# Kernel optimization log

Measured on AMD Instinct MI355X. Metric: run time of the kernel, lower is better.

The kernel has to match this reference:

```python
import jax, jax.numpy as jnp
import numpy as np

INPUT_DIM = 512
HIDDEN_DIM = 1024


def glorot_normal(key, shape):
    fan_in, fan_out = shape[0], shape[1]
    std = jnp.sqrt(2.0 / (fan_in + fan_out))
    return std * jax.random.normal(key, shape, dtype=jnp.float32)


def setup_inputs() -> dict:
    key = jax.random.key(0)
    k1, k2, k3 = jax.random.split(key, 3)
    b, t = 32, 1024
    H = HIDDEN_DIM + INPUT_DIM
    x_btd = jax.random.normal(k1, (b, t, INPUT_DIM), dtype=jnp.float32)
    input_paddings = jnp.zeros((b, t), dtype=jnp.float32)
    kernel = glorot_normal(k2, (H, 4 * HIDDEN_DIM))  # [H, 4h]
    bias = jnp.zeros((4 * HIDDEN_DIM,), dtype=jnp.float32)
    h_init = glorot_normal(k3, (1, HIDDEN_DIM))
    return {"x_btd": x_btd, "input_paddings": input_paddings,
            "kernel": kernel, "bias": bias, "h_init": h_init}


def lstm_step(carry, x_bd, kernel, bias):
    h_bh, c_bh = carry
    x_bH = jnp.concatenate([x_bd, h_bh], axis=-1)          # [b, d+h]
    gate_out = jnp.einsum('bH,Hh->bh', x_bH, kernel) + bias  # [b, 4h]
    f, i, o, g = jnp.split(gate_out, 4, axis=-1)
    c_new = jax.nn.sigmoid(f) * c_bh + jax.nn.sigmoid(i) * jnp.tanh(g)
    h_new = jax.nn.sigmoid(o) * jnp.tanh(c_new)
    return (h_new, c_new), h_new


def reference(x_btd, input_paddings, kernel, bias, h_init) -> jnp.ndarray:
    del input_paddings
    b = x_btd.shape[0]
    h0 = jnp.tile(h_init, (b, 1))                # [b, h]
    c0 = jnp.zeros((b, HIDDEN_DIM), dtype=x_btd.dtype)
    x_tbd = jnp.transpose(x_btd, (1, 0, 2))      # [t, b, d]

    def step(carry, x_bd):
        return lstm_step(carry, x_bd, kernel, bias)

    _, h_tbh = jax.lax.scan(step, (h0, c0), x_tbd)
    return jnp.transpose(h_tbh, (1, 0, 2))       # [b, t, h]
```

## Files before the change

### kernel.cpp

```cpp
#include <hip/hip_runtime.h>


#define T_STEPS 1024
#define BATCH   32
#define DIN     512
#define HID     1024
#define KTOT    1536
#define NBLK    128
#define WCOLS   32
#define WSTR    1544
#define REDSTR  33
#define REDW    (32*REDSTR)

#define LDS_W_BYTES   (WCOLS*WSTR*2)
#define LDS_RED_BYTES (4*REDW*4)
#define LDS_TOTAL     (LDS_W_BYTES + LDS_RED_BYTES)

typedef __attribute__((ext_vector_type(8))) short  short8;
typedef __attribute__((ext_vector_type(4))) float  floatx4;
typedef __attribute__((ext_vector_type(4))) unsigned short ushort4_;

__device__ __forceinline__ unsigned short f2bf(float f) {
    unsigned u = __builtin_bit_cast(unsigned, f);
    u += 0x7FFFu + ((u >> 16) & 1u);
    return (unsigned short)(u >> 16);
}
__device__ __forceinline__ float sigf(float x) { return 1.f / (1.f + __expf(-x)); }

__device__ __forceinline__ floatx4 coh_load16(const void* p) {
    floatx4 v;
    asm volatile("global_load_dwordx4 %0, %1, off sc0 sc1" : "=v"(v) : "v"(p));
    return v;
}
__device__ __forceinline__ int coh_load4(const void* p) {
    int v;
    asm volatile("global_load_dword %0, %1, off sc0 sc1\n\ts_waitcnt vmcnt(0)"
                 : "=v"(v) : "v"(p) : "memory");
    return v;
}
__device__ __forceinline__ void coh_store2(void* p, unsigned short v) {
    asm volatile("global_store_short %0, %1, off sc0 sc1" :: "v"(p), "v"((unsigned)v) : "memory");
}
__device__ __forceinline__ void coh_store4(void* p, int v) {
    asm volatile("global_store_dword %0, %1, off sc0 sc1" :: "v"(p), "v"(v) : "memory");
}
__device__ __forceinline__ void wait_vm0() {
    asm volatile("s_waitcnt vmcnt(0)" ::: "memory");
}

__global__ __launch_bounds__(256) void prep_wt(const float* __restrict__ kern,
                                               unsigned short* __restrict__ wt) {
    __shared__ unsigned short tile[64][72];
    const int c0 = (blockIdx.x & 63) * 64;
    const int k0 = (blockIdx.x >> 6) * 64;
    const int cl = threadIdx.x & 63;
    const int kg = threadIdx.x >> 6;
    #pragma unroll
    for (int i = 0; i < 16; ++i) {
        int kl = kg * 16 + i;
        tile[cl][kl] = f2bf(kern[(k0 + kl) * 4096 + c0 + cl]);
    }
    __syncthreads();
    #pragma unroll
    for (int i = 0; i < 16; ++i) {
        int cc = kg * 16 + i;
        wt[(size_t)(c0 + cc) * KTOT + k0 + cl] = tile[cc][cl];
    }
}

__global__ __launch_bounds__(256) void prep_x(const float* __restrict__ x,
                                              unsigned short* __restrict__ xT) {
    const int row = blockIdx.x * 2 + (threadIdx.x >> 7);
    const int l   = threadIdx.x & 127;
    const int b = row >> 10, t = row & 1023;
    float4 v = ((const float4*)(x + (size_t)row * DIN))[l];
    ushort4_ o;
    o.x = f2bf(v.x); o.y = f2bf(v.y); o.z = f2bf(v.z); o.w = f2bf(v.w);
    *(ushort4_*)(xT + ((size_t)t * BATCH + b) * DIN + l * 4) = o;
}

__global__ __launch_bounds__(256) void init_h(const float* __restrict__ h_init,
                                              unsigned short* __restrict__ hbuf,
                                              int* __restrict__ flags) {
    if (blockIdx.x == 32) {
        if (threadIdx.x < NBLK) flags[threadIdx.x] = 0;
        return;
    }
    const int b = blockIdx.x;
    for (int u = threadIdx.x; u < HID; u += 256)
        hbuf[b * HID + u] = f2bf(h_init[u]);
}

__global__ __launch_bounds__(256, 1) void lstm_persist(
    const unsigned short* __restrict__ wt,
    const unsigned short* __restrict__ xT,
    unsigned short* __restrict__ hbuf,
    int* __restrict__ flags,
    const float* __restrict__ bias,
    float* __restrict__ out)
{
    extern __shared__ char smem[];
    unsigned short* ldsW = (unsigned short*)smem;
    float* red = (float*)(smem + LDS_W_BYTES);

    const int bk   = blockIdx.x;
    const int tid  = threadIdx.x;
    const int wave = tid >> 6;
    const int lane = tid & 63;
    const int lrow = lane & 15;
    const int kq   = lane >> 4;

    for (int cl = wave; cl < WCOLS; cl += 4) {
        const int gcol = (cl >> 3) * HID + bk * 8 + (cl & 7);
        const unsigned short* src = wt + (size_t)gcol * KTOT;
        unsigned short* dst = ldsW + cl * WSTR;
        for (int k = lane * 8; k < KTOT; k += 512)
            *(short8*)(dst + k) = *(const short8*)(src + k);
    }

    const int pb = tid >> 3;
    const int pu = tid & 7;
    float bias_r[4];
    #pragma unroll
    for (int g = 0; g < 4; ++g) bias_r[g] = bias[g * HID + bk * 8 + pu];
    float c_state = 0.f;
    __syncthreads();

    for (int t = 0; t < T_STEPS; ++t) {
        floatx4 zero = {0.f, 0.f, 0.f, 0.f};
        floatx4 acc[2][2];
        acc[0][0] = zero; acc[0][1] = zero; acc[1][0] = zero; acc[1][1] = zero;

        const unsigned short* xb = xT + (size_t)t * (BATCH * DIN);
        #pragma unroll
        for (int i = 0; i < 4; ++i) {
            const int kl = wave * 128 + i * 32 + kq * 8;
            short8 a0 = *(const short8*)(xb + lrow * DIN + kl);
            short8 a1 = *(const short8*)(xb + (lrow + 16) * DIN + kl);
            short8 b0 = *(const short8*)(ldsW + lrow * WSTR + kl);
            short8 b1 = *(const short8*)(ldsW + (lrow + 16) * WSTR + kl);
            acc[0][0] = __builtin_amdgcn_mfma_f32_16x16x32_bf16(a0, b0, acc[0][0], 0, 0, 0);
            acc[0][1] = __builtin_amdgcn_mfma_f32_16x16x32_bf16(a0, b1, acc[0][1], 0, 0, 0);
            acc[1][0] = __builtin_amdgcn_mfma_f32_16x16x32_bf16(a1, b0, acc[1][0], 0, 0, 0);
            acc[1][1] = __builtin_amdgcn_mfma_f32_16x16x32_bf16(a1, b1, acc[1][1], 0, 0, 0);
        }

        if (t > 0 && tid < NBLK) {
            const int* fl = flags + tid;
            while (coh_load4(fl) < t)
                __builtin_amdgcn_s_sleep(1);
        }
        __syncthreads();

        const unsigned short* hb = hbuf + (size_t)(t & 1) * (BATCH * HID);
        floatx4 ha[8][2];
        #pragma unroll
        for (int i = 0; i < 8; ++i) {
            const int kh = wave * 256 + i * 32 + kq * 8;
            ha[i][0] = coh_load16(hb + lrow * HID + kh);
            ha[i][1] = coh_load16(hb + (lrow + 16) * HID + kh);
        }
        wait_vm0();
        #pragma unroll
        for (int i = 0; i < 8; ++i) {
            const int kw = 512 + wave * 256 + i * 32 + kq * 8;
            short8 a0 = __builtin_bit_cast(short8, ha[i][0]);
            short8 a1 = __builtin_bit_cast(short8, ha[i][1]);
            short8 b0 = *(const short8*)(ldsW + lrow * WSTR + kw);
            short8 b1 = *(const short8*)(ldsW + (lrow + 16) * WSTR + kw);
            acc[0][0] = __builtin_amdgcn_mfma_f32_16x16x32_bf16(a0, b0, acc[0][0], 0, 0, 0);
            acc[0][1] = __builtin_amdgcn_mfma_f32_16x16x32_bf16(a0, b1, acc[0][1], 0, 0, 0);
            acc[1][0] = __builtin_amdgcn_mfma_f32_16x16x32_bf16(a1, b0, acc[1][0], 0, 0, 0);
            acc[1][1] = __builtin_amdgcn_mfma_f32_16x16x32_bf16(a1, b1, acc[1][1], 0, 0, 0);
        }

        #pragma unroll
        for (int mt = 0; mt < 2; ++mt)
            #pragma unroll
            for (int nt = 0; nt < 2; ++nt)
                #pragma unroll
                for (int r = 0; r < 4; ++r) {
                    const int row = mt * 16 + kq * 4 + r;
                    const int col = nt * 16 + lrow;
                    red[wave * REDW + row * REDSTR + col] = acc[mt][nt][r];
                }
        __syncthreads();

        float gv[4];
        #pragma unroll
        for (int g = 0; g < 4; ++g) {
            const int col = g * 8 + pu;
            float s = bias_r[g];
            #pragma unroll
            for (int w = 0; w < 4; ++w) s += red[w * REDW + pb * REDSTR + col];
            gv[g] = s;
        }
        const float fg = sigf(gv[0]);
        const float ig = sigf(gv[1]);
        const float og = sigf(gv[2]);
        const float gg = tanhf(gv[3]);
        c_state = fg * c_state + ig * gg;
        const float hn = og * tanhf(c_state);

        out[(size_t)pb * (T_STEPS * HID) + (size_t)t * HID + bk * 8 + pu] = hn;
        unsigned short* hp = hbuf + (size_t)((t + 1) & 1) * (BATCH * HID)
                                  + pb * HID + bk * 8 + pu;
        coh_store2(hp, f2bf(hn));

        wait_vm0();
        __syncthreads();
        if (tid == 0)
            coh_store4(flags + bk, t + 1);
    }
}

extern "C" void kernel_launch(void* const* d_in, const int* in_sizes, int n_in,
                              void* d_out, int out_size, void* d_ws, size_t ws_size,
                              hipStream_t stream) {
    (void)in_sizes; (void)n_in; (void)out_size;
    const float* x      = (const float*)d_in[0];
    const float* kern   = (const float*)d_in[2];
    const float* bias   = (const float*)d_in[3];
    const float* h_init = (const float*)d_in[4];
    float* out = (float*)d_out;

    char* ws = (char*)d_ws;
    unsigned short* wt    = (unsigned short*)(ws);
    unsigned short* xT    = (unsigned short*)(ws + 12582912);
    unsigned short* hbuf  = (unsigned short*)(ws + 12582912 + 33554432);
    int*            flags = (int*)(ws + 12582912 + 33554432 + 131072);
    (void)ws_size;

    hipFuncSetAttribute((const void*)lstm_persist,
                        hipFuncAttributeMaxDynamicSharedMemorySize, LDS_TOTAL);

    prep_wt<<<dim3(64 * 24), dim3(256), 0, stream>>>(kern, wt);
    prep_x<<<dim3(BATCH * T_STEPS / 2), dim3(256), 0, stream>>>(x, xT);
    init_h<<<dim3(33), dim3(256), 0, stream>>>(h_init, hbuf, flags);

    void* args[] = { &wt, &xT, &hbuf, &flags, &bias, &out };
    hipLaunchCooperativeKernel((const void*)lstm_persist, dim3(NBLK), dim3(256),
                               args, LDS_TOTAL, stream);
}
```

Before: 5.329 ms.

## Stage h in LDS for vector stores, pad flags, per-wave flag polling

Each block now writes its new hidden-state slice into LDS, and one wave publishes it with 16-byte stores per batch row. This replaces 256 separate 2-byte coherent stores. The per-block flags are padded to a 16-byte stride. Each wave now polls only the 32 producer flags whose h slice it actually reads, which removes the block-wide barrier before the h loads. The sc0 bit is also dropped from the coherent loads and stores to use a cheaper cache scope, which carries some risk to cross-block visibility semantics.

```diff
diff --git a/kernel.cpp b/kernel.cpp
--- a/kernel.cpp
+++ b/kernel.cpp
@@ -14,7 +14,8 @@
 
 #define LDS_W_BYTES   (WCOLS*WSTR*2)
 #define LDS_RED_BYTES (4*REDW*4)
-#define LDS_TOTAL     (LDS_W_BYTES + LDS_RED_BYTES)
+#define LDS_H_BYTES   (256*2)
+#define LDS_TOTAL     (LDS_W_BYTES + LDS_RED_BYTES + LDS_H_BYTES)
 
 typedef __attribute__((ext_vector_type(8))) short  short8;
 typedef __attribute__((ext_vector_type(4))) float  floatx4;
@@ -29,20 +30,20 @@
 
 __device__ __forceinline__ floatx4 coh_load16(const void* p) {
     floatx4 v;
-    asm volatile("global_load_dwordx4 %0, %1, off sc0 sc1" : "=v"(v) : "v"(p));
+    asm volatile("global_load_dwordx4 %0, %1, off sc1" : "=v"(v) : "v"(p));
     return v;
 }
 __device__ __forceinline__ int coh_load4(const void* p) {
     int v;
-    asm volatile("global_load_dword %0, %1, off sc0 sc1\n\ts_waitcnt vmcnt(0)"
+    asm volatile("global_load_dword %0, %1, off sc1\n\ts_waitcnt vmcnt(0)"
                  : "=v"(v) : "v"(p) : "memory");
     return v;
 }
-__device__ __forceinline__ void coh_store2(void* p, unsigned short v) {
-    asm volatile("global_store_short %0, %1, off sc0 sc1" :: "v"(p), "v"((unsigned)v) : "memory");
+__device__ __forceinline__ void coh_store16(void* p, short8 v) {
+    asm volatile("global_store_dwordx4 %0, %1, off sc1" :: "v"(p), "v"(v) : "memory");
 }
 __device__ __forceinline__ void coh_store4(void* p, int v) {
-    asm volatile("global_store_dword %0, %1, off sc0 sc1" :: "v"(p), "v"(v) : "memory");
+    asm volatile("global_store_dword %0, %1, off sc1" :: "v"(p), "v"(v) : "memory");
 }
 __device__ __forceinline__ void wait_vm0() {
     asm volatile("s_waitcnt vmcnt(0)" ::: "memory");
@@ -83,7 +84,7 @@
                                               unsigned short* __restrict__ hbuf,
                                               int* __restrict__ flags) {
     if (blockIdx.x == 32) {
-        if (threadIdx.x < NBLK) flags[threadIdx.x] = 0;
+        for (int i = threadIdx.x; i < NBLK * 4; i += 256) flags[i] = 0;
         return;
     }
     const int b = blockIdx.x;
@@ -102,6 +103,7 @@
     extern __shared__ char smem[];
     unsigned short* ldsW = (unsigned short*)smem;
     float* red = (float*)(smem + LDS_W_BYTES);
+    unsigned short* hLDS = (unsigned short*)(smem + LDS_W_BYTES + LDS_RED_BYTES);
 
     const int bk   = blockIdx.x;
     const int tid  = threadIdx.x;
@@ -124,6 +126,8 @@
     #pragma unroll
     for (int g = 0; g < 4; ++g) bias_r[g] = bias[g * HID + bk * 8 + pu];
     float c_state = 0.f;
+
+    const int* myflag = flags + (wave * 32 + (lane & 31)) * 4;
     __syncthreads();
 
     for (int t = 0; t < T_STEPS; ++t) {
@@ -145,12 +149,10 @@
             acc[1][1] = __builtin_amdgcn_mfma_f32_16x16x32_bf16(a1, b1, acc[1][1], 0, 0, 0);
         }
 
-        if (t > 0 && tid < NBLK) {
-            const int* fl = flags + tid;
-            while (coh_load4(fl) < t)
+        if (t > 0) {
+            while (coh_load4(myflag) < t)
                 __builtin_amdgcn_s_sleep(1);
         }
-        __syncthreads();
 
         const unsigned short* hb = hbuf + (size_t)(t & 1) * (BATCH * HID);
         floatx4 ha[8][2];
@@ -203,14 +205,20 @@
         const float hn = og * tanhf(c_state);
 
         out[(size_t)pb * (T_STEPS * HID) + (size_t)t * HID + bk * 8 + pu] = hn;
-        unsigned short* hp = hbuf + (size_t)((t + 1) & 1) * (BATCH * HID)
-                                  + pb * HID + bk * 8 + pu;
-        coh_store2(hp, f2bf(hn));
-
-        wait_vm0();
+        hLDS[tid] = f2bf(hn);
         __syncthreads();
-        if (tid == 0)
-            coh_store4(flags + bk, t + 1);
+
+        if (wave == 0) {
+            if (lane < 32) {
+                short8 v = *(const short8*)(hLDS + lane * 8);
+                unsigned short* hp = hbuf + (size_t)((t + 1) & 1) * (BATCH * HID)
+                                          + lane * HID + bk * 8;
+                coh_store16(hp, v);
+            }
+            wait_vm0();
+            if (lane == 0)
+                coh_store4(flags + bk * 4, t + 1);
+        }
     }
 }
 
```

Result: faster. 5.020 ms (-5.8%).

## Replace per-block flag barrier with tag bits embedded in hidden-state values

Applied to the files above, without the earlier changes.

Removes the per-step flag polling and flag stores. Each bf16 hidden value now carries its LSB as a parity tag for the step, and consumers spin-reload only the h vectors whose tags do not match yet. This drops the separate flag round trip, the extra vmcnt wait before the flag store, and the s_sleep polling latency from the recurrent critical path. The cost is one bit of bf16 mantissa precision in h, plus reliance on 16-bit stores staying atomic and visible with sc1 only (sc0 is dropped). The reduction stride also changes.

```diff
diff --git a/kernel.cpp b/kernel.cpp
--- a/kernel.cpp
+++ b/kernel.cpp
@@ -9,7 +9,7 @@
 #define NBLK    128
 #define WCOLS   32
 #define WSTR    1544
-#define REDSTR  33
+#define REDSTR  35
 #define REDW    (32*REDSTR)
 
 #define LDS_W_BYTES   (WCOLS*WSTR*2)
@@ -18,6 +18,7 @@
 
 typedef __attribute__((ext_vector_type(8))) short  short8;
 typedef __attribute__((ext_vector_type(4))) float  floatx4;
+typedef __attribute__((ext_vector_type(4))) unsigned int uint4v;
 typedef __attribute__((ext_vector_type(4))) unsigned short ushort4_;
 
 __device__ __forceinline__ unsigned short f2bf(float f) {
@@ -29,20 +30,11 @@
 
 __device__ __forceinline__ floatx4 coh_load16(const void* p) {
     floatx4 v;
-    asm volatile("global_load_dwordx4 %0, %1, off sc0 sc1" : "=v"(v) : "v"(p));
+    asm volatile("global_load_dwordx4 %0, %1, off sc1" : "=v"(v) : "v"(p) : "memory");
     return v;
 }
-__device__ __forceinline__ int coh_load4(const void* p) {
-    int v;
-    asm volatile("global_load_dword %0, %1, off sc0 sc1\n\ts_waitcnt vmcnt(0)"
-                 : "=v"(v) : "v"(p) : "memory");
-    return v;
-}
 __device__ __forceinline__ void coh_store2(void* p, unsigned short v) {
-    asm volatile("global_store_short %0, %1, off sc0 sc1" :: "v"(p), "v"((unsigned)v) : "memory");
-}
-__device__ __forceinline__ void coh_store4(void* p, int v) {
-    asm volatile("global_store_dword %0, %1, off sc0 sc1" :: "v"(p), "v"(v) : "memory");
+    asm volatile("global_store_short %0, %1, off sc1" :: "v"(p), "v"((unsigned)v) : "memory");
 }
 __device__ __forceinline__ void wait_vm0() {
     asm volatile("s_waitcnt vmcnt(0)" ::: "memory");
@@ -80,22 +72,18 @@
 }
 
 __global__ __launch_bounds__(256) void init_h(const float* __restrict__ h_init,
-                                              unsigned short* __restrict__ hbuf,
-                                              int* __restrict__ flags) {
-    if (blockIdx.x == 32) {
-        if (threadIdx.x < NBLK) flags[threadIdx.x] = 0;
-        return;
-    }
+                                              unsigned short* __restrict__ hbuf) {
     const int b = blockIdx.x;
-    for (int u = threadIdx.x; u < HID; u += 256)
-        hbuf[b * HID + u] = f2bf(h_init[u]);
+    for (int u = threadIdx.x; u < HID; u += 256) {
+        hbuf[b * HID + u] = (unsigned short)(f2bf(h_init[u]) & 0xFFFEu);
+        hbuf[BATCH * HID + b * HID + u] = 0x0001;
+    }
 }
 
 __global__ __launch_bounds__(256, 1) void lstm_persist(
     const unsigned short* __restrict__ wt,
     const unsigned short* __restrict__ xT,
     unsigned short* __restrict__ hbuf,
-    int* __restrict__ flags,
     const float* __restrict__ bias,
     float* __restrict__ out)
 {
@@ -145,14 +133,9 @@
             acc[1][1] = __builtin_amdgcn_mfma_f32_16x16x32_bf16(a1, b1, acc[1][1], 0, 0, 0);
         }
 
-        if (t > 0 && tid < NBLK) {
-            const int* fl = flags + tid;
-            while (coh_load4(fl) < t)
-                __builtin_amdgcn_s_sleep(1);
-        }
-        __syncthreads();
-
         const unsigned short* hb = hbuf + (size_t)(t & 1) * (BATCH * HID);
+        const unsigned tagm = ((t >> 1) & 1) ? 0x00010001u : 0u;
+        const int tag1 = (t >> 1) & 1;
         floatx4 ha[8][2];
         #pragma unroll
         for (int i = 0; i < 8; ++i) {
@@ -161,6 +144,25 @@
             ha[i][1] = coh_load16(hb + (lrow + 16) * HID + kh);
         }
         wait_vm0();
+        for (;;) {
+            int bad = 0;
+            #pragma unroll
+            for (int i = 0; i < 8; ++i) {
+                const int kh = wave * 256 + i * 32 + kq * 8;
+                #pragma unroll
+                for (int j = 0; j < 2; ++j) {
+                    uint4v d = __builtin_bit_cast(uint4v, ha[i][j]);
+                    unsigned c = tag1 ? (d.x & d.y & d.z & d.w)
+                                      : (d.x | d.y | d.z | d.w);
+                    if ((c & 0x00010001u) != tagm) {
+                        ha[i][j] = coh_load16(hb + (lrow + j * 16) * HID + kh);
+                        bad = 1;
+                    }
+                }
+            }
+            if (!__any(bad)) break;
+            wait_vm0();
+        }
         #pragma unroll
         for (int i = 0; i < 8; ++i) {
             const int kw = 512 + wave * 256 + i * 32 + kq * 8;
@@ -202,15 +204,15 @@
         c_state = fg * c_state + ig * gg;
         const float hn = og * tanhf(c_state);
 
-        out[(size_t)pb * (T_STEPS * HID) + (size_t)t * HID + bk * 8 + pu] = hn;
+        const unsigned tagN = (unsigned)(((t + 1) >> 1) & 1);
+        unsigned short hv = (unsigned short)((f2bf(hn) & 0xFFFEu) | tagN);
         unsigned short* hp = hbuf + (size_t)((t + 1) & 1) * (BATCH * HID)
                                   + pb * HID + bk * 8 + pu;
-        coh_store2(hp, f2bf(hn));
-
-        wait_vm0();
+        coh_store2(hp, hv);
+
+        out[(size_t)pb * (T_STEPS * HID) + (size_t)t * HID + bk * 8 + pu] = hn;
+
         __syncthreads();
-        if (tid == 0)
-            coh_store4(flags + bk, t + 1);
     }
 }
 
@@ -228,7 +230,6 @@
     unsigned short* wt    = (unsigned short*)(ws);
     unsigned short* xT    = (unsigned short*)(ws + 12582912);
     unsigned short* hbuf  = (unsigned short*)(ws + 12582912 + 33554432);
-    int*            flags = (int*)(ws + 12582912 + 33554432 + 131072);
     (void)ws_size;
 
     hipFuncSetAttribute((const void*)lstm_persist,
@@ -236,9 +237,9 @@
 
     prep_wt<<<dim3(64 * 24), dim3(256), 0, stream>>>(kern, wt);
     prep_x<<<dim3(BATCH * T_STEPS / 2), dim3(256), 0, stream>>>(x, xT);
-    init_h<<<dim3(33), dim3(256), 0, stream>>>(h_init, hbuf, flags);
-
-    void* args[] = { &wt, &xT, &hbuf, &flags, &bias, &out };
+    init_h<<<dim3(32), dim3(256), 0, stream>>>(h_init, hbuf);
+
+    void* args[] = { &wt, &xT, &hbuf, &bias, &out };
     hipLaunchCooperativeKernel((const void*)lstm_persist, dim3(NBLK), dim3(256),
                                args, LDS_TOTAL, stream);
 }
```

Result: slower. 5.443 ms (+2.1%).
